# Kernel tuning notes

Hardware: AMD Instinct MI355X
Metric: run time of the kernel (lower is better)

The kernel has to match this reference:

```python
import jax, jax.numpy as jnp
import numpy as np

D = 1024      # embed_dim
H = 16        # attention heads
DH = D // H   # head size
B, S = 8, 1024
EPS = 1e-5


def setup_inputs() -> dict:
    key = jax.random.key(0)
    ks = jax.random.split(key, 12)
    s = lambda fan: 1.0 / np.sqrt(fan)
    return {
        "x":  jax.random.normal(ks[0], (B, S, D), dtype=jnp.float32),
        # per-head projections, stacked: [H, D, DH]
        "Wq": jax.random.normal(ks[1], (H, D, DH), jnp.float32) * s(D),
        "Wk": jax.random.normal(ks[2], (H, D, DH), jnp.float32) * s(D),
        "Wv": jax.random.normal(ks[3], (H, D, DH), jnp.float32) * s(D),
        "Wo": jax.random.normal(ks[4], (D, D), jnp.float32) * s(D),
        "bo": jnp.zeros((D,), jnp.float32),
        "g1": jnp.ones((D,), jnp.float32),
        "b1": jnp.zeros((D,), jnp.float32),
        "W1": jax.random.normal(ks[5], (D, 4 * D), jnp.float32) * s(D),
        "c1": jnp.zeros((4 * D,), jnp.float32),
        "W2": jax.random.normal(ks[6], (4 * D, D), jnp.float32) * s(4 * D),
        "c2": jnp.zeros((D,), jnp.float32),
        "g2": jnp.ones((D,), jnp.float32),
        "b2": jnp.zeros((D,), jnp.float32),
    }


def layer_norm(x, gain, bias):
    # torch uses unbiased variance (ddof=1)
    mean = jnp.mean(x, axis=-1, keepdims=True)
    var = jnp.var(x, axis=-1, keepdims=True, ddof=1)
    return (x - mean) / jnp.sqrt(var + EPS) * gain + bias


def reference(x, Wq, Wk, Wv, Wo, bo, g1, b1, W1, c1, W2, c2, g2, b2):
    # multi-head attention (all heads batched; same math as the per-head loop)
    q = jnp.einsum('bsd,hde->bhse', x, Wq)
    k = jnp.einsum('bsd,hde->bhse', x, Wk)
    v = jnp.einsum('bsd,hde->bhse', x, Wv)
    scores = jnp.einsum('bhse,bhte->bhst', q, k) / jnp.sqrt(jnp.float32(DH))
    attn = jax.nn.softmax(scores, axis=-1)
    ctx = jnp.einsum('bhst,bhte->bhse', attn, v)            # [B,H,S,DH]
    concat = ctx.transpose(0, 2, 1, 3).reshape(B, S, D)     # cat over heads
    attn_out = concat @ Wo + bo
    # residual + LN1
    h = layer_norm(x + attn_out, g1, b1)
    # FFN: Linear -> exact GELU -> Linear (torch nn.GELU default is erf form)
    ff = jax.nn.gelu(h @ W1 + c1, approximate=False) @ W2 + c2
    # residual + LN2
    return layer_norm(h + ff, g2, b2)
```

## Files before the change

kernel.cpp:

```cpp
#include <hip/hip_runtime.h>
#include <hip/hip_bf16.h>
#include <math.h>

typedef unsigned short u16;
typedef unsigned int u32;
typedef __attribute__((ext_vector_type(8))) __bf16 bf16x8;
typedef __attribute__((ext_vector_type(4))) float f32x4;
typedef __attribute__((ext_vector_type(16))) float f32x16;
typedef __attribute__((ext_vector_type(8))) u16 u16x8;
typedef __attribute__((ext_vector_type(4))) u16 u16x4;
typedef __attribute__((ext_vector_type(4))) u32 u32x4;

#define DEV static __device__ __forceinline__

DEV u16 f2bf(float x) {
  __bf16 b = (__bf16)x;
  return __builtin_bit_cast(u16, b);
}
DEV float bf2f(u16 u) {
  unsigned v = ((unsigned)u) << 16;
  return __builtin_bit_cast(float, v);
}

DEV void gl_lds16(const u16* g, u16* l) {
  __builtin_amdgcn_global_load_lds(
      (const __attribute__((address_space(1))) void*)g,
      (__attribute__((address_space(3))) void*)l, 16, 0, 0);
}

DEV float waveRedSum(float v) {
  v += __shfl_xor(v, 1);  v += __shfl_xor(v, 2);  v += __shfl_xor(v, 4);
  v += __shfl_xor(v, 8);  v += __shfl_xor(v, 16); v += __shfl_xor(v, 32);
  return v;
}

DEV float exp2_fast(float x) {
  float r;
  asm("v_exp_f32 %0, %1" : "=v"(r) : "v"(x));
  return r;
}
DEV float vmax16(f32x16 v) {
  float a = fmaxf(v[0], v[1]), b = fmaxf(v[2], v[3]);
  float c = fmaxf(v[4], v[5]), d = fmaxf(v[6], v[7]);
  float e = fmaxf(v[8], v[9]), f = fmaxf(v[10], v[11]);
  float g = fmaxf(v[12], v[13]), h = fmaxf(v[14], v[15]);
  a = fmaxf(a, b); c = fmaxf(c, d); e = fmaxf(e, f); g = fmaxf(g, h);
  return fmaxf(fmaxf(a, c), fmaxf(e, g));
}
DEV float vsum16(f32x16 v) {
  float a = v[0] + v[1], b = v[2] + v[3], c = v[4] + v[5], d = v[6] + v[7];
  float e = v[8] + v[9], f = v[10] + v[11], g = v[12] + v[13], h = v[14] + v[15];
  a += b; c += d; e += f; g += h;
  return (a + c) + (e + g);
}
DEV f32x16 mfma32(bf16x8 a, bf16x8 b, f32x16 c) {
  return __builtin_amdgcn_mfma_f32_32x32x16_bf16(a, b, c, 0, 0, 0);
}
DEV u32 pack2(float lo, float hi2) {
  return ((u32)f2bf(hi2) << 16) | (u32)f2bf(lo);
}
DEV void pack_direct(const f32x16& s, bf16x8* out) {
  u32x4 f0 = {pack2(s[0], s[1]),   pack2(s[2], s[3]),
              pack2(s[4], s[5]),   pack2(s[6], s[7])};
  u32x4 f1 = {pack2(s[8], s[9]),   pack2(s[10], s[11]),
              pack2(s[12], s[13]), pack2(s[14], s[15])};
  out[0] = __builtin_bit_cast(bf16x8, f0);
  out[1] = __builtin_bit_cast(bf16x8, f1);
}

__global__ __launch_bounds__(256)
void cvt_f32_bf16(const float* __restrict__ in, u16* __restrict__ out, int n8) {
  int i = blockIdx.x * 256 + threadIdx.x;
  if (i >= n8) return;
  const float4 a = *(const float4*)(in + (size_t)i * 8);
  const float4 b = *(const float4*)(in + (size_t)i * 8 + 4);
  u16x8 o;
  o[0] = f2bf(a.x); o[1] = f2bf(a.y); o[2] = f2bf(a.z); o[3] = f2bf(a.w);
  o[4] = f2bf(b.x); o[5] = f2bf(b.y); o[6] = f2bf(b.z); o[7] = f2bf(b.w);
  *(u16x8*)(out + (size_t)i * 8) = o;
}

__global__ __launch_bounds__(256)
void pack_wqkv(const float* __restrict__ Wq, const float* __restrict__ Wk,
               const float* __restrict__ Wv, u16* __restrict__ out) {
  __shared__ float tl[64][65];
  int bid = blockIdx.x;
  int which = bid / 256;
  int rem = bid % 256;
  int h = rem / 16, dt = rem % 16;
  const float* W = (which == 0) ? Wq : (which == 1) ? Wk : Wv;
  int t = threadIdx.x, tx = t & 63, ty = t >> 6;
  const float* src = W + (size_t)h * 65536 + (size_t)dt * 64 * 64;
#pragma unroll
  for (int i = 0; i < 16; ++i) {
    int dr = ty * 16 + i;
    tl[dr][tx] = src[(size_t)dr * 64 + tx];
  }
  __syncthreads();
#pragma unroll
  for (int i = 0; i < 16; ++i) {
    int e = ty * 16 + i;
    out[(size_t)(which * 1024 + h * 64 + e) * 1024 + dt * 64 + tx] = f2bf(tl[tx][e]);
  }
}

__global__ __launch_bounds__(256)
void pack_wt(const float* __restrict__ W, u16* __restrict__ out, int K, int N) {
  __shared__ float tl[64][65];
  int ntiles = N >> 6;
  int kt = blockIdx.x / ntiles, nt = blockIdx.x % ntiles;
  int t = threadIdx.x, tx = t & 63, ty = t >> 6;
#pragma unroll
  for (int i = 0; i < 16; ++i) {
    int kr = ty * 16 + i;
    tl[kr][tx] = W[(size_t)(kt * 64 + kr) * N + nt * 64 + tx];
  }
  __syncthreads();
#pragma unroll
  for (int i = 0; i < 16; ++i) {
    int nr = ty * 16 + i;
    out[(size_t)(nt * 64 + nr) * K + kt * 64 + tx] = f2bf(tl[tx][nr]);
  }
}

template <int EPI>
__global__ __launch_bounds__(512, 4)
void gemm256(const u16* __restrict__ A, const u16* __restrict__ Bt,
             void* __restrict__ Cout, const float* __restrict__ bias,
             int M, int N, int K,
             u16* __restrict__ qp_out, u16* __restrict__ kp_out,
             u16* __restrict__ vt_out) {
  constexpr int BM = 128, BN = 256;
  constexpr int SLOT = (BM + BN) * 32;
  __shared__ __align__(16) u16 lds[3 * SLOT];

  const int t = threadIdx.x;
  const int lane = t & 63, w = t >> 6;
  const int li = lane & 15, lg = lane >> 4;
  const int wm = w >> 2, wn = w & 3;

  const int tiles_n = N >> 8;
  const int nwg = gridDim.x;
  const int wgid = (blockIdx.x & 7) * (nwg >> 3) + (blockIdx.x >> 3);
  const int m0 = (wgid / tiles_n) * BM;
  const int n0 = (wgid % tiles_n) << 8;

  const int srow = t >> 2;
  const int scol = (((t & 3) ^ ((t >> 3) & 3)) << 3);
  const u16* aS0 = A  + (size_t)(m0 + srow) * K + scol;
  const u16* bS0 = Bt + (size_t)(n0 + srow) * K + scol;
  const u16* bS1 = Bt + (size_t)(n0 + 128 + srow) * K + scol;
  u16* dWave = &lds[w * 512];

  int aOff[4], bOff[4];
#pragma unroll
  for (int i = 0; i < 4; ++i) {
    int row = wm * 64 + i * 16 + li;
    aOff[i] = row * 32 + ((lg ^ ((row >> 1) & 3)) << 3);
  }
#pragma unroll
  for (int j = 0; j < 4; ++j) {
    int row = wn * 64 + j * 16 + li;
    bOff[j] = BM * 32 + row * 32 + ((lg ^ ((row >> 1) & 3)) << 3);
  }

  f32x4 acc[4][4] = {};
  const int NT = K >> 5;

#define STAGE256(TT, SL)                                             \
  {                                                                  \
    const int kk = (TT) << 5;                                        \
    u16* db = dWave + (SL) * SLOT;                                   \
    gl_lds16(aS0 + kk, db);                                          \
    gl_lds16(bS0 + kk, db + BM * 32);                                \
    gl_lds16(bS1 + kk, db + BM * 32 + 4096);                         \
  }

  STAGE256(0, 0);
  STAGE256(1, 1);

  int so = 0;
  for (int tt = 0; tt < NT; ++tt) {
    int s2 = so + 2; if (s2 >= 3) s2 -= 3;
    if (tt + 2 < NT) {
      STAGE256(tt + 2, s2);
      asm volatile("s_waitcnt vmcnt(6)" ::: "memory");
    } else if (tt + 1 < NT) {
      asm volatile("s_waitcnt vmcnt(3)" ::: "memory");
    } else {
      asm volatile("s_waitcnt vmcnt(0)" ::: "memory");
    }
    __builtin_amdgcn_s_barrier();
    __builtin_amdgcn_sched_barrier(0);

    const u16* sb = &lds[so * SLOT];
    bf16x8 af[4], bfr[4];
#pragma unroll
    for (int i = 0; i < 4; ++i) af[i] = *(const bf16x8*)&sb[aOff[i]];
#pragma unroll
    for (int j = 0; j < 4; ++j) bfr[j] = *(const bf16x8*)&sb[bOff[j]];

    __builtin_amdgcn_s_setprio(1);
#pragma unroll
    for (int i = 0; i < 4; ++i)
#pragma unroll
      for (int j = 0; j < 4; ++j)
        acc[i][j] = __builtin_amdgcn_mfma_f32_16x16x32_bf16(af[i], bfr[j], acc[i][j], 0, 0, 0);
    __builtin_amdgcn_s_setprio(0);

    __builtin_amdgcn_sched_barrier(0);
    __builtin_amdgcn_s_barrier();
    so = (so + 1 == 3) ? 0 : so + 1;
  }
#undef STAGE256

  if constexpr (EPI == 3) {
    const int which = n0 >> 10;
    const int colb = (n0 & 1023) + wn * 64 + li;
#pragma unroll
    for (int i = 0; i < 4; ++i) {
      const int row0 = m0 + wm * 64 + i * 16 + lg * 4;
      const int bb = row0 >> 10;
      const int s0r = row0 & 1023;
#pragma unroll
      for (int j = 0; j < 4; ++j) {
        const int c = colb + j * 16;
        const int hh = c >> 6, e = c & 63;
        const size_t hb = ((size_t)(bb * 16 + hh)) << 16;
        if (which == 2) {
          u16x4 pk;
#pragma unroll
          for (int r = 0; r < 4; ++r) pk[r] = f2bf(acc[i][j][r]);
          const int s_sw = (s0r & ~12) | ((s0r & 4) << 1) | ((s0r & 8) >> 1);
          *(u16x4*)(vt_out + hb + ((size_t)e << 10) + s_sw) = pk;
        } else {
          u16* dst = (which == 0) ? qp_out : kp_out;
#pragma unroll
          for (int r = 0; r < 4; ++r)
            dst[hb + (size_t)(s0r + r) * 64 + e] = f2bf(acc[i][j][r]);
        }
      }
    }
    return;
  }

  const int colBase = n0 + wn * 64 + li;
#pragma unroll
  for (int i = 0; i < 4; ++i) {
#pragma unroll
    for (int j = 0; j < 4; ++j) {
      int col = colBase + j * 16;
      float bv = bias[col];
#pragma unroll
      for (int r = 0; r < 4; ++r) {
        int row = m0 + wm * 64 + i * 16 + lg * 4 + r;
        float v = acc[i][j][r] + bv;
        if (EPI == 2) v = 0.5f * v * (1.0f + erff(v * 0.70710678118654752f));
        if (EPI == 1) ((float*)Cout)[(size_t)row * N + col] = v;
        else          ((u16*)Cout)[(size_t)row * N + col] = f2bf(v);
      }
    }
  }
}

__global__ __launch_bounds__(256, 2)
void attn32(const u16* __restrict__ qp, const u16* __restrict__ kp,
            const u16* __restrict__ vt, u16* __restrict__ ctx) {
  __shared__ __align__(16) u16 lds[2][2][4096];
  const int t = threadIdx.x, l = t & 63, w = t >> 6;
  const int l31 = l & 31, hi = l >> 5;
  const int bid = blockIdx.x;
  const int idx = bid >> 3;
  const int bh = (bid & 7) * 16 + (idx >> 3);
  const int qt = idx & 7;
  const int b = bh >> 4, h = bh & 15;
  const int qg = qt * 128 + w * 32;
  const size_t base = (size_t)bh << 16;
  const float SC = 0.18033688011112042f;

  const u16* qrow = qp + base + (size_t)(qg + l31) * 64 + 8 * hi;
  bf16x8 qb[4];
#pragma unroll
  for (int f = 0; f < 4; ++f) qb[f] = *(const bf16x8*)(qrow + f * 16);

  const u16* kbh = kp + base;
  const u16* vbh = vt + base;
  const int sl0 = w, sl1 = 4 + w;

#define STAGE_KV(KB, BUF)                                                        \
  {                                                                              \
    u16* KT = &lds[BUF][0][0];                                                   \
    u16* VT = &lds[BUF][1][0];                                                   \
    const u16* ks = kbh + (size_t)(KB) * 4096;                                   \
    const u16* vs = vbh + (KB) * 64;                                             \
    gl_lds16(ks + (size_t)l * 64 + sl0 * 8,   KT + sl0 * 512);                   \
    gl_lds16(ks + (size_t)l * 64 + sl1 * 8,   KT + sl1 * 512);                   \
    gl_lds16(vs + (size_t)l * 1024 + sl0 * 8, VT + sl0 * 512);                   \
    gl_lds16(vs + (size_t)l * 1024 + sl1 * 8, VT + sl1 * 512);                   \
  }

  f32x16 o0 = {}, o1 = {};
  float m_run = -1e30f, l_run = 0.0f;

  STAGE_KV(0, 0);
  __syncthreads();

  int buf = 0;
  for (int kb = 0; kb < 16; ++kb) {
    if (kb < 15) STAGE_KV(kb + 1, buf ^ 1);

    const u16* KT = &lds[buf][0][0];
    const u16* VT = &lds[buf][1][0];

    bf16x8 ka[8];
#pragma unroll
    for (int f = 0; f < 4; ++f) {
      const int s = (2 * f + hi) * 512 + l31 * 8;
      ka[f]     = *(const bf16x8*)&KT[s];
      ka[4 + f] = *(const bf16x8*)&KT[s + 256];
    }

    __builtin_amdgcn_s_setprio(1);
    f32x16 s0 = {}, s1 = {};
#pragma unroll
    for (int f = 0; f < 4; ++f) s0 = mfma32(ka[f], qb[f], s0);
#pragma unroll
    for (int f = 0; f < 4; ++f) s1 = mfma32(ka[4 + f], qb[f], s1);
    __builtin_amdgcn_s_setprio(0);

    bf16x8 va[8];
#pragma unroll
    for (int c = 0; c < 4; ++c) {
      const int s = (2 * c + hi) * 512 + l31 * 8;
      va[c]     = *(const bf16x8*)&VT[s];
      va[4 + c] = *(const bf16x8*)&VT[s + 256];
    }

    s0 *= SC; s1 *= SC;

    float mx = fmaxf(vmax16(s0), vmax16(s1));
    mx = fmaxf(mx, __shfl_xor(mx, 32));

    float mn = fmaxf(m_run, mx);
    float al = exp2_fast(m_run - mn);
    m_run = mn;
    l_run *= al; o0 *= al; o1 *= al;

#pragma unroll
    for (int i = 0; i < 16; ++i) s0[i] = exp2_fast(s0[i] - m_run);
#pragma unroll
    for (int i = 0; i < 16; ++i) s1[i] = exp2_fast(s1[i] - m_run);

    float sm = vsum16(s0) + vsum16(s1);
    sm += __shfl_xor(sm, 32);
    l_run += sm;

    bf16x8 pb[4];
    pack_direct(s0, &pb[0]);
    pack_direct(s1, &pb[2]);

    __builtin_amdgcn_s_setprio(1);
    o0 = mfma32(va[0], pb[0], o0);
    o0 = mfma32(va[1], pb[1], o0);
    o0 = mfma32(va[2], pb[2], o0);
    o0 = mfma32(va[3], pb[3], o0);
    o1 = mfma32(va[4], pb[0], o1);
    o1 = mfma32(va[5], pb[1], o1);
    o1 = mfma32(va[6], pb[2], o1);
    o1 = mfma32(va[7], pb[3], o1);
    __builtin_amdgcn_s_setprio(0);

    __syncthreads();
    buf ^= 1;
  }
#undef STAGE_KV

  float inv = 1.0f / l_run;
  o0 *= inv; o1 *= inv;
  u16* crow = ctx + (size_t)(b * 1024 + qg + l31) * 1024 + h * 64 + 4 * hi;
#pragma unroll
  for (int g = 0; g < 4; ++g) {
    u16x4 p0, p1;
#pragma unroll
    for (int j = 0; j < 4; ++j) { p0[j] = f2bf(o0[g * 4 + j]); p1[j] = f2bf(o1[g * 4 + j]); }
    *(u16x4*)(crow + g * 8) = p0;
    *(u16x4*)(crow + 32 + g * 8) = p1;
  }
}

template <int MODE>
__global__ __launch_bounds__(256)
void ln_kernel(const void* __restrict__ in1v, const float* __restrict__ in2,
               const float* __restrict__ g, const float* __restrict__ bt,
               void* __restrict__ outv) {
  __shared__ float red[4];
  const int row = blockIdx.x;
  const int t = threadIdx.x;
  const int c = t * 4;
  const size_t base = (size_t)row * 1024 + c;

  float a0, a1, a2, a3;
  {
    const float4 y = *(const float4*)(in2 + base);
    if (MODE == 0) {
      const float4 x = *(const float4*)((const float*)in1v + base);
      a0 = x.x + y.x; a1 = x.y + y.y; a2 = x.z + y.z; a3 = x.w + y.w;
    } else {
      u16x4 xb = *(const u16x4*)((const u16*)in1v + base);
      a0 = bf2f(xb[0]) + y.x; a1 = bf2f(xb[1]) + y.y;
      a2 = bf2f(xb[2]) + y.z; a3 = bf2f(xb[3]) + y.w;
    }
  }
  float sum = waveRedSum(a0 + a1 + a2 + a3);
  if ((t & 63) == 0) red[t >> 6] = sum;
  __syncthreads();
  float mean = (red[0] + red[1] + red[2] + red[3]) * (1.0f / 1024.0f);
  __syncthreads();
  float d0 = a0 - mean, d1 = a1 - mean, d2 = a2 - mean, d3 = a3 - mean;
  float sq = waveRedSum(d0 * d0 + d1 * d1 + d2 * d2 + d3 * d3);
  if ((t & 63) == 0) red[t >> 6] = sq;
  __syncthreads();
  float var = (red[0] + red[1] + red[2] + red[3]) * (1.0f / 1023.0f);
  float inv = rsqrtf(var + 1e-5f);
  const float4 gv = *(const float4*)(g + c);
  const float4 bv = *(const float4*)(bt + c);
  float o0 = d0 * inv * gv.x + bv.x;
  float o1 = d1 * inv * gv.y + bv.y;
  float o2 = d2 * inv * gv.z + bv.z;
  float o3 = d3 * inv * gv.w + bv.w;
  if (MODE == 0) {
    u16x4 ob; ob[0] = f2bf(o0); ob[1] = f2bf(o1); ob[2] = f2bf(o2); ob[3] = f2bf(o3);
    *(u16x4*)((u16*)outv + base) = ob;
  } else {
    float4 of; of.x = o0; of.y = o1; of.z = o2; of.w = o3;
    *(float4*)((float*)outv + base) = of;
  }
}

extern "C" void kernel_launch(void* const* d_in, const int* in_sizes, int n_in,
                              void* d_out, int out_size, void* d_ws, size_t ws_size,
                              hipStream_t stream) {
  const float* x  = (const float*)d_in[0];
  const float* Wq = (const float*)d_in[1];
  const float* Wk = (const float*)d_in[2];
  const float* Wv = (const float*)d_in[3];
  const float* Wo = (const float*)d_in[4];
  const float* bo = (const float*)d_in[5];
  const float* g1 = (const float*)d_in[6];
  const float* b1 = (const float*)d_in[7];
  const float* W1 = (const float*)d_in[8];
  const float* c1 = (const float*)d_in[9];
  const float* W2 = (const float*)d_in[10];
  const float* c2 = (const float*)d_in[11];
  const float* g2 = (const float*)d_in[12];
  const float* b2 = (const float*)d_in[13];
  float* out = (float*)d_out;

  char* ws = (char*)d_ws;
  u16* xb     = (u16*)(ws + 0);
  u16* wqkv_b = (u16*)(ws + 16777216);
  u16* wo_b   = (u16*)(ws + 23068672);
  u16* w1_b   = (u16*)(ws + 25165824);
  u16* w2_b   = (u16*)(ws + 33554432);
  char* R1 = ws + 41943040;
  u16*  qpb  = (u16*)(R1);
  u16*  kpb  = (u16*)(R1 + 16777216);
  u16*  vtb  = (u16*)(R1 + 33554432);
  u16*  ctx  = (u16*)(R1 + 50331648);
  float* attn = (float*)(R1 + 67108864);
  u16*  ff1  = (u16*)(R1);
  float* ff2 = (float*)(R1 + 67108864);
  u16*  h_b  = xb;

  cvt_f32_bf16<<<4096, 256, 0, stream>>>(x, xb, 1048576);
  pack_wqkv<<<768, 256, 0, stream>>>(Wq, Wk, Wv, wqkv_b);
  pack_wt<<<256, 256, 0, stream>>>(Wo, wo_b, 1024, 1024);
  pack_wt<<<1024, 256, 0, stream>>>(W1, w1_b, 1024, 4096);
  pack_wt<<<1024, 256, 0, stream>>>(W2, w2_b, 4096, 1024);

  gemm256<3><<<768, 512, 0, stream>>>(xb, wqkv_b, nullptr, nullptr,
                                      8192, 3072, 1024, qpb, kpb, vtb);
  attn32<<<1024, 256, 0, stream>>>(qpb, kpb, vtb, ctx);
  gemm256<1><<<256, 512, 0, stream>>>(ctx, wo_b, attn, bo, 8192, 1024, 1024,
                                      nullptr, nullptr, nullptr);
  ln_kernel<0><<<8192, 256, 0, stream>>>(x, attn, g1, b1, h_b);
  gemm256<2><<<1024, 512, 0, stream>>>(h_b, w1_b, ff1, c1, 8192, 4096, 1024,
                                       nullptr, nullptr, nullptr);
  gemm256<1><<<256, 512, 0, stream>>>(ff1, w2_b, ff2, c2, 8192, 1024, 4096,
                                      nullptr, nullptr, nullptr);
  ln_kernel<1><<<8192, 256, 0, stream>>>(h_b, ff2, g2, b2, out);
}
```

Before: 364.3 us.

## Add 256x256-tile double-buffered GEMM for QKV and FFN1 projections

Introduces a gemm512 kernel with a 256x256 output tile (each wave computes 128x64) and a two-slot LDS double buffer whose global-to-LDS loads are interleaved across four MFMA phases with partial vmcnt waits. It is used for the QKV projection and the first FFN GEMM, halving the grid size. The aim is more arithmetic per loaded byte and better hiding of load latency in the two largest GEMMs. The larger tile doubles accumulator registers and LDS per block, which lowers occupancy (launch bounds 2), and the smaller grid may leave fewer waves to fill the GPU. The QKV-scatter epilogue is removed from gemm256 because that kernel is no longer used for QKV.

```diff
diff --git a/kernel.cpp b/kernel.cpp
--- a/kernel.cpp
+++ b/kernel.cpp
@@ -124,6 +124,160 @@
 }
 
 template <int EPI>
+__global__ __launch_bounds__(512, 2)
+void gemm512(const u16* __restrict__ A, const u16* __restrict__ Bt,
+             void* __restrict__ Cout, const float* __restrict__ bias,
+             int M, int N, int K,
+             u16* __restrict__ qp_out, u16* __restrict__ kp_out,
+             u16* __restrict__ vt_out) {
+  constexpr int QSZ = 4096;
+  constexpr int MATSZ = 4 * QSZ;
+  constexpr int DBSZ = 2 * MATSZ;
+  __shared__ __align__(16) u16 lds[2 * DBSZ];
+
+  const int t = threadIdx.x;
+  const int lane = t & 63, w = t >> 6;
+  const int li = lane & 15, lg = lane >> 4;
+  const int wm = w >> 2, wn = w & 3;
+
+  const int tiles_n = N >> 8;
+  const int nwg = gridDim.x;
+  const int wgid = (blockIdx.x & 7) * (nwg >> 3) + (blockIdx.x >> 3);
+  const int m0 = (wgid / tiles_n) << 8;
+  const int n0 = (wgid % tiles_n) << 8;
+
+  const int sr = t >> 3, cs = t & 7;
+  const int kk = ((cs ^ sr) & 7) << 3;
+  const u16* aSrc = A + (size_t)(m0 + sr) * K + kk;
+  const u16* bSrc = Bt + (size_t)(n0 + sr) * K + kk;
+  u16* dBase = &lds[w * 512];
+
+  int aOf[2][4], bOf[4];
+#pragma unroll
+  for (int ms = 0; ms < 2; ++ms)
+#pragma unroll
+    for (int ii = 0; ii < 4; ++ii) {
+      int r = wm * 128 + ms * 64 + ii * 16 + li;
+      aOf[ms][ii] = r * 64 + (((lg ^ r) & 7) << 3);
+    }
+#pragma unroll
+  for (int j = 0; j < 4; ++j) {
+    int r = wn * 64 + j * 16 + li;
+    bOf[j] = MATSZ + r * 64 + (((lg ^ r) & 7) << 3);
+  }
+
+  f32x4 acc[8][4] = {};
+  const int NT = K >> 6;
+
+#define STG_A(Q, TT, DB) gl_lds16(aSrc + (size_t)(Q) * 64 * K + (size_t)(TT) * 64, \
+                                  dBase + (DB) * DBSZ + (Q) * QSZ)
+#define STG_B(Q, TT, DB) gl_lds16(bSrc + (size_t)(Q) * 64 * K + (size_t)(TT) * 64, \
+                                  dBase + (DB) * DBSZ + MATSZ + (Q) * QSZ)
+
+#define PHASE_MFMA(MS, KHX)                                                     \
+  {                                                                             \
+    bf16x8 af_[4];                                                              \
+    _Pragma("unroll") for (int ii = 0; ii < 4; ++ii)                            \
+        af_[ii] = *(const bf16x8*)&sa[aOf[MS][ii] ^ (KHX)];                     \
+    __builtin_amdgcn_s_setprio(1);                                              \
+    _Pragma("unroll") for (int ii = 0; ii < 4; ++ii)                            \
+      _Pragma("unroll") for (int j = 0; j < 4; ++j)                             \
+          acc[(MS)*4 + ii][j] = __builtin_amdgcn_mfma_f32_16x16x32_bf16(        \
+              af_[ii], bf[j], acc[(MS)*4 + ii][j], 0, 0, 0);                    \
+    __builtin_amdgcn_s_setprio(0);                                              \
+  }
+
+#pragma unroll
+  for (int q = 0; q < 4; ++q) { STG_A(q, 0, 0); STG_B(q, 0, 0); }
+  asm volatile("s_waitcnt vmcnt(0)" ::: "memory");
+  __builtin_amdgcn_s_barrier();
+  __builtin_amdgcn_sched_barrier(0);
+
+  for (int tt = 0; tt < NT; ++tt) {
+    const int d = tt & 1, dn = d ^ 1;
+    const u16* sa = &lds[d * DBSZ];
+    const bool more = (tt + 1) < NT;
+
+    if (more) { STG_B(0, tt + 1, dn); STG_B(1, tt + 1, dn); STG_A(0, tt + 1, dn); }
+    bf16x8 bf[4];
+#pragma unroll
+    for (int j = 0; j < 4; ++j) bf[j] = *(const bf16x8*)&sa[bOf[j]];
+    PHASE_MFMA(0, 0)
+    __builtin_amdgcn_sched_barrier(0);
+    if (more) asm volatile("s_waitcnt vmcnt(3)" ::: "memory");
+    else      asm volatile("s_waitcnt vmcnt(0)" ::: "memory");
+    __builtin_amdgcn_s_barrier();
+    __builtin_amdgcn_sched_barrier(0);
+
+    if (more) { STG_B(2, tt + 1, dn); STG_B(3, tt + 1, dn); STG_A(2, tt + 1, dn); }
+    PHASE_MFMA(1, 0)
+
+    if (more) { STG_A(1, tt + 1, dn); STG_A(3, tt + 1, dn); }
+#pragma unroll
+    for (int j = 0; j < 4; ++j) bf[j] = *(const bf16x8*)&sa[bOf[j] ^ 32];
+    PHASE_MFMA(0, 32)
+
+    PHASE_MFMA(1, 32)
+    __builtin_amdgcn_sched_barrier(0);
+    if (more) asm volatile("s_waitcnt vmcnt(2)" ::: "memory");
+    else      asm volatile("s_waitcnt vmcnt(0)" ::: "memory");
+    __builtin_amdgcn_s_barrier();
+    __builtin_amdgcn_sched_barrier(0);
+  }
+#undef STG_A
+#undef STG_B
+#undef PHASE_MFMA
+
+  if constexpr (EPI == 3) {
+    const int which = n0 >> 10;
+    const int colb = (n0 & 1023) + wn * 64 + li;
+#pragma unroll
+    for (int i = 0; i < 8; ++i) {
+      const int row0 = m0 + wm * 128 + i * 16 + lg * 4;
+      const int bb = row0 >> 10;
+      const int s0r = row0 & 1023;
+#pragma unroll
+      for (int j = 0; j < 4; ++j) {
+        const int c = colb + j * 16;
+        const int hh = c >> 6, e = c & 63;
+        const size_t hb = ((size_t)(bb * 16 + hh)) << 16;
+        if (which == 2) {
+          u16x4 pk;
+#pragma unroll
+          for (int r = 0; r < 4; ++r) pk[r] = f2bf(acc[i][j][r]);
+          const int s_sw = (s0r & ~12) | ((s0r & 4) << 1) | ((s0r & 8) >> 1);
+          *(u16x4*)(vt_out + hb + ((size_t)e << 10) + s_sw) = pk;
+        } else {
+          u16* dst = (which == 0) ? qp_out : kp_out;
+#pragma unroll
+          for (int r = 0; r < 4; ++r)
+            dst[hb + (size_t)(s0r + r) * 64 + e] = f2bf(acc[i][j][r]);
+        }
+      }
+    }
+    return;
+  }
+
+  const int colBase = n0 + wn * 64 + li;
+#pragma unroll
+  for (int i = 0; i < 8; ++i) {
+#pragma unroll
+    for (int j = 0; j < 4; ++j) {
+      int col = colBase + j * 16;
+      float bv = bias[col];
+#pragma unroll
+      for (int r = 0; r < 4; ++r) {
+        int row = m0 + wm * 128 + i * 16 + lg * 4 + r;
+        float v = acc[i][j][r] + bv;
+        if (EPI == 2) v = 0.5f * v * (1.0f + erff(v * 0.70710678118654752f));
+        if (EPI == 1) ((float*)Cout)[(size_t)row * N + col] = v;
+        else          ((u16*)Cout)[(size_t)row * N + col] = f2bf(v);
+      }
+    }
+  }
+}
+
+template <int EPI>
 __global__ __launch_bounds__(512, 4)
 void gemm256(const u16* __restrict__ A, const u16* __restrict__ Bt,
              void* __restrict__ Cout, const float* __restrict__ bias,
@@ -213,36 +367,6 @@
     so = (so + 1 == 3) ? 0 : so + 1;
   }
 #undef STAGE256
-
-  if constexpr (EPI == 3) {
-    const int which = n0 >> 10;
-    const int colb = (n0 & 1023) + wn * 64 + li;
-#pragma unroll
-    for (int i = 0; i < 4; ++i) {
-      const int row0 = m0 + wm * 64 + i * 16 + lg * 4;
-      const int bb = row0 >> 10;
-      const int s0r = row0 & 1023;
-#pragma unroll
-      for (int j = 0; j < 4; ++j) {
-        const int c = colb + j * 16;
-        const int hh = c >> 6, e = c & 63;
-        const size_t hb = ((size_t)(bb * 16 + hh)) << 16;
-        if (which == 2) {
-          u16x4 pk;
-#pragma unroll
-          for (int r = 0; r < 4; ++r) pk[r] = f2bf(acc[i][j][r]);
-          const int s_sw = (s0r & ~12) | ((s0r & 4) << 1) | ((s0r & 8) >> 1);
-          *(u16x4*)(vt_out + hb + ((size_t)e << 10) + s_sw) = pk;
-        } else {
-          u16* dst = (which == 0) ? qp_out : kp_out;
-#pragma unroll
-          for (int r = 0; r < 4; ++r)
-            dst[hb + (size_t)(s0r + r) * 64 + e] = f2bf(acc[i][j][r]);
-        }
-      }
-    }
-    return;
-  }
 
   const int colBase = n0 + wn * 64 + li;
 #pragma unroll
@@ -478,14 +602,14 @@
   pack_wt<<<1024, 256, 0, stream>>>(W1, w1_b, 1024, 4096);
   pack_wt<<<1024, 256, 0, stream>>>(W2, w2_b, 4096, 1024);
 
-  gemm256<3><<<768, 512, 0, stream>>>(xb, wqkv_b, nullptr, nullptr,
+  gemm512<3><<<384, 512, 0, stream>>>(xb, wqkv_b, nullptr, nullptr,
                                       8192, 3072, 1024, qpb, kpb, vtb);
   attn32<<<1024, 256, 0, stream>>>(qpb, kpb, vtb, ctx);
   gemm256<1><<<256, 512, 0, stream>>>(ctx, wo_b, attn, bo, 8192, 1024, 1024,
                                       nullptr, nullptr, nullptr);
   ln_kernel<0><<<8192, 256, 0, stream>>>(x, attn, g1, b1, h_b);
-  gemm256<2><<<1024, 512, 0, stream>>>(h_b, w1_b, ff1, c1, 8192, 4096, 1024,
-                                       nullptr, nullptr, nullptr);
+  gemm512<2><<<512, 512, 0, stream>>>(h_b, w1_b, ff1, c1, 8192, 4096, 1024,
+                                      nullptr, nullptr, nullptr);
   gemm256<1><<<256, 512, 0, stream>>>(ff1, w2_b, ff2, c2, 8192, 1024, 4096,
                                       nullptr, nullptr, nullptr);
   ln_kernel<1><<<8192, 256, 0, stream>>>(h_b, ff2, g2, b2, out);
```

Result: no change. 371.2 us (+1.9%).
